# Optimization experiments

Measured on AMD Instinct MI355X. Metric: run time of the kernel, lower is better.

The kernel has to match this reference:

```python
import jax, jax.numpy as jnp
import numpy as np

D_MODEL = 256
D_STATE = 64
NGROUPS = 2
EXPAND = 4
HEADDIM = 128
D_CONV = 4
D_INNER = EXPAND * D_MODEL              # 1024
NHEADS = D_INNER // HEADDIM             # 8
GN = NGROUPS * D_STATE                  # 128
D_IN_PROJ = 2 * D_INNER + 2 * GN + NHEADS  # 2312
EPS = 1e-5


def setup_inputs() -> dict:
    key = jax.random.key(0)
    ks = jax.random.split(key, 12)
    B, L = 2, 4096
    u = jax.random.normal(ks[0], (B, L, D_MODEL), dtype=jnp.float32)
    ln_gamma = jnp.ones((D_MODEL,), jnp.float32)
    ln_beta = jnp.zeros((D_MODEL,), jnp.float32)
    W_in = jax.random.normal(ks[1], (D_MODEL, D_IN_PROJ), jnp.float32) / np.sqrt(D_MODEL)
    conv_w = jax.random.normal(ks[2], (D_INNER + 2 * GN, D_CONV), jnp.float32) * 0.2
    conv_b = jax.random.normal(ks[3], (D_INNER + 2 * GN,), jnp.float32) * 0.02
    dt_bias = jnp.log(jnp.expm1(jax.random.uniform(ks[4], (NHEADS,), jnp.float32, 0.001, 0.1)))
    A_log = jnp.log(jax.random.uniform(ks[5], (NHEADS,), jnp.float32, 1.0, 16.0))
    D_param = jnp.ones((NHEADS,), jnp.float32)
    B_head_scale = jnp.ones((NHEADS, GN), jnp.float32) + 0.02 * jax.random.normal(ks[6], (NHEADS, GN), jnp.float32)
    rms_weight = jnp.ones((D_INNER,), jnp.float32)
    W_out = jax.random.normal(ks[7], (D_INNER, D_MODEL), jnp.float32) / np.sqrt(D_INNER)
    return dict(u=u, ln_gamma=ln_gamma, ln_beta=ln_beta, W_in=W_in, conv_w=conv_w,
                conv_b=conv_b, dt_bias=dt_bias, A_log=A_log, D_param=D_param,
                B_head_scale=B_head_scale, rms_weight=rms_weight, W_out=W_out)


def _mamba_mes(xn, W_in, conv_w, conv_b, dt_bias, A_log, D_param, B_head_scale, rms_weight, W_out):
    B, L, _ = xn.shape
    H, P, K = NHEADS, HEADDIM, D_CONV
    zxbcdt = xn @ W_in                                   # (B,L,2312)
    z = zxbcdt[..., :D_INNER]
    xBC = zxbcdt[..., D_INNER:D_INNER + D_INNER + 2 * GN]
    dt = zxbcdt[..., -H:]
    dt_pos = jax.nn.softplus(dt + dt_bias)               # (B,L,H)
    # causal depthwise conv1d + silu
    xp = jnp.pad(xBC, ((0, 0), (K - 1, 0), (0, 0)))
    conv = sum(xp[:, k:k + L, :] * conv_w[:, k] for k in range(K)) + conv_b
    xBC = jax.nn.silu(conv)
    x = xBC[..., :D_INNER]
    B_shared = xBC[..., D_INNER:D_INNER + GN]            # (B,L,GN)
    C_shared = xBC[..., D_INNER + GN:]                   # (B,L,GN)
    # MES: per-head B via diagonal scale, shared x (mean over heads) and shared C
    B_h = B_shared[:, :, None, :] * B_head_scale[None, None]          # (B,L,H,GN)
    x_shared = x.reshape(B, L, H, P).mean(axis=2)                     # (B,L,P)
    A = -jnp.exp(A_log)                                               # (H,)
    dA = jnp.exp(dt_pos * A)                                          # (B,L,H)
    # selective scan; per-head state (GN, P)
    def step(state, inp):
        dA_t, dt_t, B_t, C_t, x_t = inp   # (B,H),(B,H),(B,H,GN),(B,GN),(B,P)
        state = dA_t[:, :, None, None] * state + jnp.einsum('bh,bhn,bp->bhnp', dt_t, B_t, x_t)
        y_t = jnp.einsum('bn,bhnp->bhp', C_t, state)
        return state, y_t
    init = jnp.zeros((B, H, GN, P), xn.dtype)
    xs = (jnp.moveaxis(dA, 1, 0), jnp.moveaxis(dt_pos, 1, 0), jnp.moveaxis(B_h, 1, 0),
          jnp.moveaxis(C_shared, 1, 0), jnp.moveaxis(x_shared, 1, 0))
    _, ys = jax.lax.scan(step, init, xs)
    y = jnp.moveaxis(ys, 0, 1)                                        # (B,L,H,P)
    y = y + D_param[None, None, :, None] * x_shared[:, :, None, :]    # skip term D*x
    y = y.reshape(B, L, D_INNER)
    # gated RMSNorm: y * silu(z), then rmsnorm
    yg = y * jax.nn.silu(z)
    y = yg * jax.lax.rsqrt(jnp.mean(yg * yg, axis=-1, keepdims=True) + EPS) * rms_weight
    return y @ W_out


def reference(u, ln_gamma, ln_beta, W_in, conv_w, conv_b, dt_bias, A_log,
              D_param, B_head_scale, rms_weight, W_out):
    # pre-LayerNorm
    mu = jnp.mean(u, axis=-1, keepdims=True)
    var = jnp.mean((u - mu) ** 2, axis=-1, keepdims=True)
    xn = (u - mu) * jax.lax.rsqrt(var + EPS) * ln_gamma + ln_beta
    out = _mamba_mes(xn, W_in, conv_w, conv_b, dt_bias, A_log, D_param,
                     B_head_scale, rms_weight, W_out)
    return u + out  # dropout is identity in eval
```

## Files before the change

### kernel.cpp

```cpp
#include <hip/hip_runtime.h>
#include <math.h>

#define LN_TOK 4096
#define NB 2
#define NROWS (NB * LN_TOK)
#define DMODEL 256
#define DINNER 1024
#define NHEADS 8
#define GNN 128
#define DPROJ 2312
#define ZSTRIDE 2432
#define EPSF 1e-5f
#define NCHUNK 32
#define CHUNK 128
#define APAD 72
#define BPAD 64
#define MPAD 136
#define TT 16

typedef unsigned short u16;
typedef unsigned int u32;
typedef __attribute__((ext_vector_type(8))) short shortx8;
typedef __attribute__((ext_vector_type(4))) float floatx4;

__device__ __forceinline__ float sigmoidf_(float v) { return 1.f / (1.f + __expf(-v)); }
__device__ __forceinline__ float siluf_(float v)    { return v / (1.f + __expf(-v)); }
__device__ __forceinline__ float softplusf_(float v){ return v > 20.f ? v : log1pf(__expf(v)); }
__device__ __forceinline__ float b2f(u16 h) { return __uint_as_float(((u32)h) << 16); }
__device__ __forceinline__ u16 f2b(float f) {
    u32 u = __float_as_uint(f);
    u32 r = (u + 0x7fffu + ((u >> 16) & 1u)) >> 16;
    return (u16)r;
}
__device__ __forceinline__ void gld16(const void* g, void* l) {
    __builtin_amdgcn_global_load_lds((const __attribute__((address_space(1))) unsigned int*)g,
                                     (__attribute__((address_space(3))) unsigned int*)l, 16, 0, 0);
}

__global__ __launch_bounds__(256) void k_prologue(const float* __restrict__ u,
                                                  const float* __restrict__ gam,
                                                  const float* __restrict__ bet,
                                                  u16* __restrict__ xn,
                                                  const float* __restrict__ W_in,
                                                  u16* __restrict__ Wt,
                                                  const float* __restrict__ W_out,
                                                  u16* __restrict__ Wot) {
    __shared__ float smem[64 * 65];
    int bid = blockIdx.x;
    int tid = threadIdx.x;
    if (bid < NROWS) {
        float v = u[(size_t)bid * DMODEL + tid];
        float* s1 = smem;
        float* s2 = smem + 256;
        s1[tid] = v; s2[tid] = v * v;
        __syncthreads();
        for (int off = 128; off > 0; off >>= 1) {
            if (tid < off) { s1[tid] += s1[tid + off]; s2[tid] += s2[tid + off]; }
            __syncthreads();
        }
        float mean = s1[0] * (1.f / DMODEL);
        float var  = s2[0] * (1.f / DMODEL) - mean * mean;
        float r = rsqrtf(var + EPSF);
        xn[(size_t)bid * DMODEL + tid] = f2b((v - mean) * r * gam[tid] + bet[tid]);
    } else {
        const float* in; u16* outp; int R, C, Cp, gx, gy;
        if (bid < NROWS + 152) {
            int q = bid - NROWS;
            in = W_in; outp = Wt; R = DMODEL; C = DPROJ; Cp = ZSTRIDE;
            gx = q % (ZSTRIDE / 64); gy = q / (ZSTRIDE / 64);
        } else {
            int q = bid - NROWS - 152;
            in = W_out; outp = Wot; R = DINNER; C = DMODEL; Cp = DMODEL;
            gx = q % (DMODEL / 64); gy = q / (DMODEL / 64);
        }
        float (*tile)[65] = (float(*)[65])smem;
        int c0 = gx * 64, r0 = gy * 64;
        int tx = tid & 63, ty = tid >> 6;
        for (int rr = ty; rr < 64; rr += 4) {
            int r = r0 + rr, c = c0 + tx;
            tile[rr][tx] = (r < R && c < C) ? in[(size_t)r * C + c] : 0.f;
        }
        __syncthreads();
        for (int cc = ty; cc < 64; cc += 4) {
            int c = c0 + cc, r = r0 + tx;
            if (c < Cp && r < R) outp[(size_t)c * R + r] = f2b(tile[tx][cc]);
        }
    }
}

__global__ __launch_bounds__(256) void k_gemm_bf(const u16* __restrict__ A,
                                                 const u16* __restrict__ Bt,
                                                 u16* __restrict__ C,
                                                 int K, int ldc) {
    __shared__ u16 As[128 * BPAD];
    __shared__ u16 Bs[128 * BPAD];
    int tid = threadIdx.x;
    int wave = tid >> 6, lane = tid & 63;
    int wm = wave >> 1, wn = wave & 1;
    int quad = lane >> 4, l16 = lane & 15;
    int m0 = blockIdx.y * 128, n0 = blockIdx.x * 128;
    floatx4 acc[4][4] = {};
    for (int k0 = 0; k0 < K; k0 += 64) {
#pragma unroll
        for (int p = 0; p < 4; p++) {
            int i = p * 256 + tid;
            int row = i >> 3, kk = (i & 7) << 3;
            gld16(&A[(size_t)(m0 + row) * K + k0 + kk], &As[i * 8]);
            gld16(&Bt[(size_t)(n0 + row) * K + k0 + kk], &Bs[i * 8]);
        }
        __syncthreads();
#pragma unroll
        for (int ks = 0; ks < 64; ks += 32) {
            shortx8 af[4], bfr[4];
#pragma unroll
            for (int i = 0; i < 4; i++)
                af[i] = *(shortx8*)&As[(wm * 64 + i * 16 + l16) * BPAD + ks + (quad << 3)];
#pragma unroll
            for (int j = 0; j < 4; j++)
                bfr[j] = *(shortx8*)&Bs[(wn * 64 + j * 16 + l16) * BPAD + ks + (quad << 3)];
#pragma unroll
            for (int i = 0; i < 4; i++)
#pragma unroll
                for (int j = 0; j < 4; j++)
                    acc[i][j] = __builtin_amdgcn_mfma_f32_16x16x32_bf16(af[i], bfr[j], acc[i][j], 0, 0, 0);
        }
        __syncthreads();
    }
#pragma unroll
    for (int i = 0; i < 4; i++) {
        int row = m0 + wm * 64 + i * 16 + quad * 4;
#pragma unroll
        for (int j = 0; j < 4; j++) {
            int col = n0 + wn * 64 + j * 16 + l16;
#pragma unroll
            for (int r = 0; r < 4; r++)
                C[(size_t)(row + r) * ldc + col] = f2b(acc[i][j][r]);
        }
    }
}

__global__ __launch_bounds__(256) void k_gemm2(const u16* __restrict__ A,
                                               const u16* __restrict__ Bt,
                                               float* __restrict__ C,
                                               int K, int ldc,
                                               const float* __restrict__ addC) {
    __shared__ u16 As[128 * BPAD];
    __shared__ u16 Bs[64 * BPAD];
    int tid = threadIdx.x;
    int wave = tid >> 6, lane = tid & 63;
    int wm = wave >> 1, wn = wave & 1;
    int quad = lane >> 4, l16 = lane & 15;
    int m0 = blockIdx.y * 128, n0 = blockIdx.x * 64;
    floatx4 acc[4][2] = {};
    for (int k0 = 0; k0 < K; k0 += 64) {
#pragma unroll
        for (int p = 0; p < 4; p++) {
            int i = p * 256 + tid;
            int row = i >> 3, kk = (i & 7) << 3;
            gld16(&A[(size_t)(m0 + row) * K + k0 + kk], &As[i * 8]);
        }
#pragma unroll
        for (int p = 0; p < 2; p++) {
            int i = p * 256 + tid;
            int row = i >> 3, kk = (i & 7) << 3;
            gld16(&Bt[(size_t)(n0 + row) * K + k0 + kk], &Bs[i * 8]);
        }
        __syncthreads();
#pragma unroll
        for (int ks = 0; ks < 64; ks += 32) {
            shortx8 af[4], bfr[2];
#pragma unroll
            for (int i = 0; i < 4; i++)
                af[i] = *(shortx8*)&As[(wm * 64 + i * 16 + l16) * BPAD + ks + (quad << 3)];
#pragma unroll
            for (int j = 0; j < 2; j++)
                bfr[j] = *(shortx8*)&Bs[(wn * 32 + j * 16 + l16) * BPAD + ks + (quad << 3)];
#pragma unroll
            for (int i = 0; i < 4; i++)
#pragma unroll
                for (int j = 0; j < 2; j++)
                    acc[i][j] = __builtin_amdgcn_mfma_f32_16x16x32_bf16(af[i], bfr[j], acc[i][j], 0, 0, 0);
        }
        __syncthreads();
    }
#pragma unroll
    for (int i = 0; i < 4; i++) {
        int row = m0 + wm * 64 + i * 16 + quad * 4;
#pragma unroll
        for (int j = 0; j < 2; j++) {
            int col = n0 + wn * 32 + j * 16 + l16;
#pragma unroll
            for (int r = 0; r < 4; r++) {
                size_t idx = (size_t)(row + r) * ldc + col;
                float v = acc[i][j][r];
                if (addC) v += addC[idx];
                C[idx] = v;
            }
        }
    }
}

#define LDW 1296
__global__ __launch_bounds__(256) void k_conv(const u16* __restrict__ zxb,
                                              const float* __restrict__ cw,
                                              const float* __restrict__ cb,
                                              const float* __restrict__ dt_bias,
                                              const float* __restrict__ A_log,
                                              u16* __restrict__ xsh, u16* __restrict__ Bsh,
                                              u16* __restrict__ Csh, u16* __restrict__ XT,
                                              u16* __restrict__ BT,
                                              float* __restrict__ dtp, float* __restrict__ laa) {
    int blk = blockIdx.x;
    int b = blk / (LN_TOK / TT), tile = blk % (LN_TOK / TT);
    int t0 = tile * TT;
    int tid = threadIdx.x;
    __shared__ u16 ld[(TT + 3) * LDW];
    __shared__ float sv[TT][260];
    __shared__ u16 bcv[TT][132];

    for (int i = tid; i < (TT + 3) * 161; i += 256) {
        int r = i / 161, ch = (i % 161) * 8;
        int t = t0 - 3 + r;
        int4 v = make_int4(0, 0, 0, 0);
        if (t >= 0)
            v = *(const int4*)&zxb[((size_t)(b * LN_TOK + t)) * ZSTRIDE + DINNER + ch];
        *(int4*)&ld[r * LDW + ch] = v;
    }

    int cmap[5];
#pragma unroll
    for (int k = 0; k < 4; k++) cmap[k] = (tid >> 7) * 512 + (tid & 127) + 128 * k;
    cmap[4] = 1024 + tid;
    float w0[5], w1[5], w2[5], w3[5], bias[5];
#pragma unroll
    for (int k = 0; k < 5; k++) {
        int c = cmap[k];
        w0[k] = cw[c * 4 + 0]; w1[k] = cw[c * 4 + 1];
        w2[k] = cw[c * 4 + 2]; w3[k] = cw[c * 4 + 3];
        bias[k] = cb[c];
    }
    float dtb = 0.f, negA = 0.f;
    if (tid < NHEADS) { dtb = dt_bias[tid]; negA = -__expf(A_log[tid]); }

    __syncthreads();

    float h1[5], h2[5], h3[5];
#pragma unroll
    for (int k = 0; k < 5; k++) {
        h3[k] = b2f(ld[0 * LDW + cmap[k]]);
        h2[k] = b2f(ld[1 * LDW + cmap[k]]);
        h1[k] = b2f(ld[2 * LDW + cmap[k]]);
    }

    for (int m = 0; m < TT; m++) {
        int t = t0 + m;
        size_t rowp = (size_t)(b * LN_TOK + t) * GNN;
        float xpart = 0.f;
#pragma unroll
        for (int k = 0; k < 5; k++) {
            float cur = b2f(ld[(m + 3) * LDW + cmap[k]]);
            float conv = bias[k] + w3[k] * cur + w2[k] * h1[k] + w1[k] * h2[k] + w0[k] * h3[k];
            h3[k] = h2[k]; h2[k] = h1[k]; h1[k] = cur;
            float s = siluf_(conv);
            if (k < 4) xpart += s;
            else {
                u16 sb = f2b(s);
                if (tid < 128) { Bsh[rowp + tid] = sb; bcv[m][tid] = sb; }
                else           Csh[rowp + tid - 128] = sb;
            }
        }
        sv[m][tid] = xpart;
        if (tid < NHEADS) {
            float dtv = b2f(ld[(m + 3) * LDW + 1280 + tid]) + dtb;
            float dp = softplusf_(dtv);
            size_t idx = ((size_t)(b * NHEADS + tid)) * LN_TOK + t;
            dtp[idx] = dp;
            laa[idx] = negA * dp;
        }
    }
    __syncthreads();

    for (int idx = tid; idx < TT * 128; idx += 256) {
        int m = idx >> 7, p = idx & 127;
        xsh[(size_t)(b * LN_TOK + t0 + m) * GNN + p] =
            f2b((sv[m][p] + sv[m][p + 128]) * 0.125f);
    }
    {
        int p = tid & 127, tg = tid >> 7;
        u16 ox[8], ob[8];
#pragma unroll
        for (int j = 0; j < 8; j++) {
            int m = tg * 8 + j;
            ox[j] = f2b((sv[m][p] + sv[m][p + 128]) * 0.125f);
            ob[j] = bcv[m][p];
        }
        size_t base = ((size_t)(b * GNN + p)) * LN_TOK + t0 + tg * 8;
        int4 vx = make_int4((u32)ox[0] | ((u32)ox[1] << 16), (u32)ox[2] | ((u32)ox[3] << 16),
                            (u32)ox[4] | ((u32)ox[5] << 16), (u32)ox[6] | ((u32)ox[7] << 16));
        int4 vb = make_int4((u32)ob[0] | ((u32)ob[1] << 16), (u32)ob[2] | ((u32)ob[3] << 16),
                            (u32)ob[4] | ((u32)ob[5] << 16), (u32)ob[6] | ((u32)ob[7] << 16));
        *(int4*)&XT[base] = vx;
        *(int4*)&BT[base] = vb;
    }
}

__global__ __launch_bounds__(256) void k_chunkS(const u16* __restrict__ BT,
                                                const u16* __restrict__ XT,
                                                const float* __restrict__ scale,
                                                const float* __restrict__ laa,
                                                const float* __restrict__ dtp,
                                                u16* __restrict__ states,
                                                float* __restrict__ gtot) {
    int blk = blockIdx.x;
    int c = blk & 31, h = (blk >> 5) & 7, b = blk >> 8;
    int t0 = c * CHUNK;
    __shared__ u16 As[128 * APAD];
    __shared__ u16 Bs[128 * BPAD];
    __shared__ float g[128], esc[128], scl[128];
    int tid = threadIdx.x;
    int wave = tid >> 6, lane = tid & 63;
    int wm = wave >> 1, wn = wave & 1;
    int quad = lane >> 4, l16 = lane & 15;
    size_t bhbase = (size_t)(b * NHEADS + h) * LN_TOK + t0;
    if (tid < 128) g[tid] = laa[bhbase + tid];
    __syncthreads();
#pragma unroll
    for (int off = 1; off < 128; off <<= 1) {
        float v = 0.f;
        if (tid < 128 && tid >= off) v = g[tid - off];
        __syncthreads();
        if (tid < 128) g[tid] += v;
        __syncthreads();
    }
    if (tid < 128) {
        esc[tid] = __expf(g[127] - g[tid]) * dtp[bhbase + tid];
        scl[tid] = scale[h * GNN + tid];
    }
    if (tid == 0) gtot[(size_t)(b * NHEADS + h) * NCHUNK + c] = g[127];
    __syncthreads();
    floatx4 acc[4][4] = {};
    size_t tbase = (size_t)(b * GNN) * LN_TOK + t0;
    for (int k0 = 0; k0 < 128; k0 += 64) {
#pragma unroll
        for (int p = 0; p < 4; p++) {
            int i = p * 256 + tid;
            int row = i >> 3, kk = (i & 7) << 3;
            gld16(&XT[tbase + (size_t)row * LN_TOK + k0 + kk], &Bs[i * 8]);
            int4 raw = *(const int4*)&BT[tbase + (size_t)row * LN_TOK + k0 + kk];
            u16* rp = (u16*)&raw;
            float sr = scl[row];
            u32 w[4];
#pragma unroll
            for (int q = 0; q < 4; q++) {
                u16 a  = f2b(b2f(rp[2 * q])     * sr * esc[k0 + kk + 2 * q]);
                u16 bb = f2b(b2f(rp[2 * q + 1]) * sr * esc[k0 + kk + 2 * q + 1]);
                w[q] = (u32)a | ((u32)bb << 16);
            }
            *(int4*)&As[row * APAD + kk] = make_int4(w[0], w[1], w[2], w[3]);
        }
        __syncthreads();
#pragma unroll
        for (int ks = 0; ks < 64; ks += 32) {
            shortx8 af[4], bfr[4];
#pragma unroll
            for (int i = 0; i < 4; i++)
                af[i] = *(shortx8*)&As[(wm * 64 + i * 16 + l16) * APAD + ks + (quad << 3)];
#pragma unroll
            for (int j = 0; j < 4; j++)
                bfr[j] = *(shortx8*)&Bs[(wn * 64 + j * 16 + l16) * BPAD + ks + (quad << 3)];
#pragma unroll
            for (int i = 0; i < 4; i++)
#pragma unroll
                for (int j = 0; j < 4; j++)
                    acc[i][j] = __builtin_amdgcn_mfma_f32_16x16x32_bf16(af[i], bfr[j], acc[i][j], 0, 0, 0);
        }
        __syncthreads();
    }
    size_t sbase = (size_t)blk * 16384;
#pragma unroll
    for (int i = 0; i < 4; i++) {
        int n0 = wm * 64 + i * 16 + quad * 4;
#pragma unroll
        for (int j = 0; j < 4; j++) {
            int p = wn * 64 + j * 16 + l16;
            u16 o[4];
#pragma unroll
            for (int r = 0; r < 4; r++) o[r] = f2b(acc[i][j][r]);
            u32 lo = (u32)o[0] | ((u32)o[1] << 16);
            u32 hi = (u32)o[2] | ((u32)o[3] << 16);
            *(uint2*)&states[sbase + (size_t)p * CHUNK + n0] = make_uint2(lo, hi);
        }
    }
}

__global__ void k_scan(u16* __restrict__ states, const float* __restrict__ gtot) {
    int idx = blockIdx.x * 256 + threadIdx.x;
    int bh = idx >> 13;
    int np = (idx & 8191) * 2;
    __shared__ float sG[NCHUNK];
    if (threadIdx.x < NCHUNK) sG[threadIdx.x] = __expf(gtot[bh * NCHUNK + threadIdx.x]);
    __syncthreads();
    size_t base = (size_t)bh * NCHUNK * 16384 + np;
    float r0 = 0.f, r1 = 0.f;
    u32 v = *(u32*)&states[base];
    for (int c = 0; c < NCHUNK; c++) {
        u32 vn = (c < NCHUNK - 1) ? *(u32*)&states[base + (size_t)(c + 1) * 16384] : 0u;
        float l0 = b2f((u16)(v & 0xffff)), l1 = b2f((u16)(v >> 16));
        *(u32*)&states[base + (size_t)c * 16384] = (u32)f2b(r0) | ((u32)f2b(r1) << 16);
        float G = sG[c];
        r0 = G * r0 + l0; r1 = G * r1 + l1;
        v = vn;
    }
}

__global__ __launch_bounds__(256) void k_chunkMY2(const u16* __restrict__ Bsh,
                                                  const u16* __restrict__ Csh,
                                                  const float* __restrict__ scale,
                                                  const u16* __restrict__ states,
                                                  const u16* __restrict__ XT,
                                                  const float* __restrict__ laa,
                                                  const float* __restrict__ dtp,
                                                  u16* __restrict__ y) {
    int blk = blockIdx.x;
    int c = blk & 31, h = (blk >> 5) & 7, b = blk >> 8;
    int t0 = c * CHUNK;
    __shared__ u16 MtAs[128 * MPAD];
    __shared__ u16 Bs[128 * BPAD];
    __shared__ float gsh[128], eg[128], dts[128], sc[128];
    int tid = threadIdx.x;
    int wave = tid >> 6, lane = tid & 63;
    int wm = wave >> 1, wn = wave & 1;
    int quad = lane >> 4, l16 = lane & 15;
    size_t bhbase = (size_t)(b * NHEADS + h) * LN_TOK + t0;
    if (tid < 128) gsh[tid] = laa[bhbase + tid];
    __syncthreads();
#pragma unroll
    for (int off = 1; off < 128; off <<= 1) {
        float v = 0.f;
        if (tid < 128 && tid >= off) v = gsh[tid - off];
        __syncthreads();
        if (tid < 128) gsh[tid] += v;
        __syncthreads();
    }
    if (tid < 128) {
        eg[tid] = __expf(gsh[tid]);
        dts[tid] = dtp[bhbase + tid];
        sc[tid] = scale[h * GNN + tid];
    }
    __syncthreads();
    floatx4 acc[4][4] = {};
    size_t rbase = (size_t)(b * LN_TOK + t0) * GNN;
    for (int k0 = 0; k0 < 128; k0 += 64) {
#pragma unroll
        for (int p = 0; p < 4; p++) {
            int i = p * 256 + tid;
            int row = i >> 3, kk = (i & 7) << 3;
            gld16(&Csh[rbase + (size_t)row * GNN + k0 + kk], &Bs[i * 8]);
            int4 raw = *(const int4*)&Bsh[rbase + (size_t)row * GNN + k0 + kk];
            u16* rp = (u16*)&raw;
            u32 w[4];
#pragma unroll
            for (int q = 0; q < 4; q++) {
                u16 a  = f2b(b2f(rp[2 * q])     * sc[k0 + kk + 2 * q]);
                u16 bb = f2b(b2f(rp[2 * q + 1]) * sc[k0 + kk + 2 * q + 1]);
                w[q] = (u32)a | ((u32)bb << 16);
            }
            *(int4*)&MtAs[row * APAD + kk] = make_int4(w[0], w[1], w[2], w[3]);
        }
        __syncthreads();
#pragma unroll
        for (int ks = 0; ks < 64; ks += 32) {
            shortx8 af[4], bfr[4];
#pragma unroll
            for (int i = 0; i < 4; i++)
                af[i] = *(shortx8*)&MtAs[(wm * 64 + i * 16 + l16) * APAD + ks + (quad << 3)];
#pragma unroll
            for (int j = 0; j < 4; j++)
                bfr[j] = *(shortx8*)&Bs[(wn * 64 + j * 16 + l16) * BPAD + ks + (quad << 3)];
#pragma unroll
            for (int i = 0; i < 4; i++)
#pragma unroll
                for (int j = 0; j < 4; j++)
                    acc[i][j] = __builtin_amdgcn_mfma_f32_16x16x32_bf16(af[i], bfr[j], acc[i][j], 0, 0, 0);
        }
        __syncthreads();
    }
#pragma unroll
    for (int i = 0; i < 4; i++) {
        int s0 = wm * 64 + i * 16 + quad * 4;
#pragma unroll
        for (int j = 0; j < 4; j++) {
            int t = wn * 64 + j * 16 + l16;
            u16 o[4];
#pragma unroll
            for (int r = 0; r < 4; r++) {
                int s = s0 + r;
                float v = (s <= t) ? acc[i][j][r] * __expf(gsh[t] - gsh[s]) * dts[s] : 0.f;
                o[r] = f2b(v);
            }
            u32 lo = (u32)o[0] | ((u32)o[1] << 16);
            u32 hi = (u32)o[2] | ((u32)o[3] << 16);
            *(uint2*)&MtAs[t * MPAD + s0] = make_uint2(lo, hi);
            acc[i][j] = (floatx4){0.f, 0.f, 0.f, 0.f};
        }
    }
    __syncthreads();
    size_t xtb = (size_t)(b * GNN) * LN_TOK + t0;
    for (int k0 = 0; k0 < 128; k0 += 64) {
#pragma unroll
        for (int p = 0; p < 4; p++) {
            int i = p * 256 + tid;
            int row = i >> 3, kk = (i & 7) << 3;
            gld16(&XT[xtb + (size_t)row * LN_TOK + k0 + kk], &Bs[i * 8]);
        }
        __syncthreads();
#pragma unroll
        for (int ks = 0; ks < 64; ks += 32) {
            shortx8 af[4], bfr[4];
#pragma unroll
            for (int i = 0; i < 4; i++)
                af[i] = *(shortx8*)&MtAs[(wm * 64 + i * 16 + l16) * MPAD + k0 + ks + (quad << 3)];
#pragma unroll
            for (int j = 0; j < 4; j++)
                bfr[j] = *(shortx8*)&Bs[(wn * 64 + j * 16 + l16) * BPAD + ks + (quad << 3)];
#pragma unroll
            for (int i = 0; i < 4; i++)
#pragma unroll
                for (int j = 0; j < 4; j++)
                    acc[i][j] = __builtin_amdgcn_mfma_f32_16x16x32_bf16(af[i], bfr[j], acc[i][j], 0, 0, 0);
        }
        __syncthreads();
    }
    size_t sbase = (size_t)blk * 16384;
    for (int k0 = 0; k0 < 128; k0 += 64) {
#pragma unroll
        for (int p = 0; p < 4; p++) {
            int i = p * 256 + tid;
            int row = i >> 3, kk = (i & 7) << 3;
            gld16(&states[sbase + (size_t)row * CHUNK + k0 + kk], &Bs[i * 8]);
            int4 raw = *(const int4*)&Csh[rbase + (size_t)row * GNN + k0 + kk];
            float e = eg[row];
            u16* rp = (u16*)&raw;
            u32 w[4];
#pragma unroll
            for (int q = 0; q < 4; q++) {
                u16 a  = f2b(b2f(rp[2 * q]) * e);
                u16 bb = f2b(b2f(rp[2 * q + 1]) * e);
                w[q] = (u32)a | ((u32)bb << 16);
            }
            *(int4*)&MtAs[row * APAD + kk] = make_int4(w[0], w[1], w[2], w[3]);
        }
        __syncthreads();
#pragma unroll
        for (int ks = 0; ks < 64; ks += 32) {
            shortx8 af[4], bfr[4];
#pragma unroll
            for (int i = 0; i < 4; i++)
                af[i] = *(shortx8*)&MtAs[(wm * 64 + i * 16 + l16) * APAD + ks + (quad << 3)];
#pragma unroll
            for (int j = 0; j < 4; j++)
                bfr[j] = *(shortx8*)&Bs[(wn * 64 + j * 16 + l16) * BPAD + ks + (quad << 3)];
#pragma unroll
            for (int i = 0; i < 4; i++)
#pragma unroll
                for (int j = 0; j < 4; j++)
                    acc[i][j] = __builtin_amdgcn_mfma_f32_16x16x32_bf16(af[i], bfr[j], acc[i][j], 0, 0, 0);
        }
        __syncthreads();
    }
#pragma unroll
    for (int i = 0; i < 4; i++) {
        int t = wm * 64 + i * 16 + quad * 4;
#pragma unroll
        for (int j = 0; j < 4; j++) {
            int p = wn * 64 + j * 16 + l16;
#pragma unroll
            for (int r = 0; r < 4; r++)
                y[((size_t)(b * LN_TOK + t0 + t + r)) * DINNER + h * GNN + p] = f2b(acc[i][j][r]);
        }
    }
}

__global__ void k_gate(const u16* __restrict__ y, const u16* __restrict__ zxb,
                       const u16* __restrict__ xsh, const float* __restrict__ Dp,
                       const float* __restrict__ rw, u16* __restrict__ ybuf) {
    int row = blockIdx.x;
    int tid = threadIdx.x;
    size_t yb = (size_t)row * DINNER;
    size_t zb = (size_t)row * ZSTRIDE;
    size_t xb = (size_t)row * GNN;
    float yg[4];
    float ss = 0.f;
#pragma unroll
    for (int q = 0; q < 4; q++) {
        int k = tid * 4 + q;
        int h = k >> 7, p = k & 127;
        float z = b2f(zxb[zb + k]);
        float v = (b2f(y[yb + k]) + Dp[h] * b2f(xsh[xb + p])) * z * sigmoidf_(z);
        yg[q] = v;
        ss += v * v;
    }
    __shared__ float red[256];
    red[tid] = ss;
    __syncthreads();
    for (int off = 128; off > 0; off >>= 1) {
        if (tid < off) red[tid] += red[tid + off];
        __syncthreads();
    }
    float scale = rsqrtf(red[0] * (1.f / DINNER) + EPSF);
#pragma unroll
    for (int q = 0; q < 4; q++) {
        int k = tid * 4 + q;
        ybuf[yb + k] = f2b(yg[q] * scale * rw[k]);
    }
}

extern "C" void kernel_launch(void* const* d_in, const int* in_sizes, int n_in,
                              void* d_out, int out_size, void* d_ws, size_t ws_size,
                              hipStream_t stream) {
    (void)in_sizes; (void)n_in; (void)out_size; (void)ws_size;
    const float* u        = (const float*)d_in[0];
    const float* ln_gamma = (const float*)d_in[1];
    const float* ln_beta  = (const float*)d_in[2];
    const float* W_in     = (const float*)d_in[3];
    const float* conv_w   = (const float*)d_in[4];
    const float* conv_b   = (const float*)d_in[5];
    const float* dt_bias  = (const float*)d_in[6];
    const float* A_log    = (const float*)d_in[7];
    const float* D_param  = (const float*)d_in[8];
    const float* B_scale  = (const float*)d_in[9];
    const float* rms_w    = (const float*)d_in[10];
    const float* W_out    = (const float*)d_in[11];
    float* out = (float*)d_out;

    char* ws = (char*)d_ws;
    u16*   xn_b   = (u16*)ws;                 ws += (size_t)NROWS * DMODEL * 2;
    u16*   Wt     = (u16*)ws;                 ws += (size_t)ZSTRIDE * DMODEL * 2;
    u16*   Wot    = (u16*)ws;                 ws += (size_t)DMODEL * DINNER * 2;
    u16*   zxb    = (u16*)ws;                 ws += (size_t)NROWS * ZSTRIDE * 2;
    u16*   xsh    = (u16*)ws;                 ws += (size_t)NROWS * GNN * 2;
    u16*   Bsh    = (u16*)ws;                 ws += (size_t)NROWS * GNN * 2;
    u16*   Csh    = (u16*)ws;                 ws += (size_t)NROWS * GNN * 2;
    u16*   XT     = (u16*)ws;                 ws += (size_t)NB * GNN * LN_TOK * 2;
    u16*   BT     = (u16*)ws;                 ws += (size_t)NB * GNN * LN_TOK * 2;
    float* dtp    = (float*)ws;               ws += (size_t)NB * NHEADS * LN_TOK * 4;
    float* laa    = (float*)ws;               ws += (size_t)NB * NHEADS * LN_TOK * 4;
    float* gtot   = (float*)ws;               ws += (size_t)NB * NHEADS * NCHUNK * 4;
    u16*   states = (u16*)ws;                 ws += (size_t)512 * 16384 * 2;
    u16*   ybig   = (u16*)ws;                 ws += (size_t)NROWS * DINNER * 2;
    u16*   ybuf   = (u16*)ws;                 ws += (size_t)NROWS * DINNER * 2;

    k_prologue<<<NROWS + 152 + 64, 256, 0, stream>>>(u, ln_gamma, ln_beta, xn_b,
                                                     W_in, Wt, W_out, Wot);

    k_gemm_bf<<<dim3(ZSTRIDE / 128, NROWS / 128), 256, 0, stream>>>(xn_b, Wt, zxb, DMODEL, ZSTRIDE);

    k_conv<<<NROWS / TT, 256, 0, stream>>>(zxb, conv_w, conv_b, dt_bias, A_log,
                                           xsh, Bsh, Csh, XT, BT, dtp, laa);

    k_chunkS<<<NB * NHEADS * NCHUNK, 256, 0, stream>>>(BT, XT, B_scale, laa, dtp, states, gtot);

    k_scan<<<512, 256, 0, stream>>>(states, gtot);

    k_chunkMY2<<<NB * NHEADS * NCHUNK, 256, 0, stream>>>(Bsh, Csh, B_scale, states,
                                                         XT, laa, dtp, ybig);

    k_gate<<<NROWS, 256, 0, stream>>>(ybig, zxb, xsh, D_param, rms_w, ybuf);

    k_gemm2<<<dim3(DMODEL / 64, NROWS / 128), 256, 0, stream>>>(ybuf, Wot, out, DINNER, DMODEL, u);
}
```

Baseline: 215.0 us.

## Load full 128-wide K tiles at once and use wave-shuffle prefix scan in chunk kernels

In k_chunkS and k_chunkMY2 each GEMM stage now stages the whole 128-wide K dimension in shared memory in one pass, replacing two 64-wide passes. This removes the per-half barriers and the reload loop, at the cost of more LDS per block, which can lower occupancy. The 128-element cumulative log-decay scan, which used a barrier per step, is replaced by a 64-lane __shfl_up scan per wavefront plus one shared-memory carry. A few barriers between phases are also moved or dropped.

```diff
diff --git a/kernel.cpp b/kernel.cpp
--- a/kernel.cpp
+++ b/kernel.cpp
@@ -13,9 +13,9 @@
 #define EPSF 1e-5f
 #define NCHUNK 32
 #define CHUNK 128
-#define APAD 72
 #define BPAD 64
-#define MPAD 136
+#define FPAD 136
+#define BKF 128
 #define TT 16
 
 typedef unsigned short u16;
@@ -314,67 +314,69 @@
     int blk = blockIdx.x;
     int c = blk & 31, h = (blk >> 5) & 7, b = blk >> 8;
     int t0 = c * CHUNK;
-    __shared__ u16 As[128 * APAD];
-    __shared__ u16 Bs[128 * BPAD];
-    __shared__ float g[128], esc[128], scl[128];
+    __shared__ u16 As[128 * FPAD];
+    __shared__ u16 Bs[128 * BKF];
+    __shared__ float gsh[132], esc[128], scl[128];
     int tid = threadIdx.x;
     int wave = tid >> 6, lane = tid & 63;
     int wm = wave >> 1, wn = wave & 1;
     int quad = lane >> 4, l16 = lane & 15;
     size_t bhbase = (size_t)(b * NHEADS + h) * LN_TOK + t0;
-    if (tid < 128) g[tid] = laa[bhbase + tid];
-    __syncthreads();
-#pragma unroll
-    for (int off = 1; off < 128; off <<= 1) {
-        float v = 0.f;
-        if (tid < 128 && tid >= off) v = g[tid - off];
-        __syncthreads();
-        if (tid < 128) g[tid] += v;
-        __syncthreads();
-    }
+
+    float gv = (tid < 128) ? laa[bhbase + tid] : 0.f;
+#pragma unroll
+    for (int off = 1; off < 64; off <<= 1) {
+        float v = __shfl_up(gv, off, 64);
+        if (lane >= off) gv += v;
+    }
+    if (tid == 63) gsh[130] = gv;
+    __syncthreads();
+    if (tid >= 64 && tid < 128) gv += gsh[130];
+    if (tid < 128) gsh[tid] = gv;
+    __syncthreads();
+    float glast = gsh[127];
     if (tid < 128) {
-        esc[tid] = __expf(g[127] - g[tid]) * dtp[bhbase + tid];
+        esc[tid] = __expf(glast - gsh[tid]) * dtp[bhbase + tid];
         scl[tid] = scale[h * GNN + tid];
     }
-    if (tid == 0) gtot[(size_t)(b * NHEADS + h) * NCHUNK + c] = g[127];
-    __syncthreads();
+    if (tid == 0) gtot[(size_t)(b * NHEADS + h) * NCHUNK + c] = glast;
+    __syncthreads();
+
+    size_t tbase = (size_t)(b * GNN) * LN_TOK + t0;
+#pragma unroll
+    for (int p = 0; p < 8; p++) {
+        int i = p * 256 + tid;
+        int row = i >> 4, kk = (i & 15) << 3;
+        gld16(&XT[tbase + (size_t)row * LN_TOK + kk], &Bs[i * 8]);
+        int4 raw = *(const int4*)&BT[tbase + (size_t)row * LN_TOK + kk];
+        u16* rp = (u16*)&raw;
+        float sr = scl[row];
+        u32 w[4];
+#pragma unroll
+        for (int q = 0; q < 4; q++) {
+            u16 a  = f2b(b2f(rp[2 * q])     * sr * esc[kk + 2 * q]);
+            u16 bb = f2b(b2f(rp[2 * q + 1]) * sr * esc[kk + 2 * q + 1]);
+            w[q] = (u32)a | ((u32)bb << 16);
+        }
+        *(int4*)&As[row * FPAD + kk] = make_int4(w[0], w[1], w[2], w[3]);
+    }
+    __syncthreads();
+
     floatx4 acc[4][4] = {};
-    size_t tbase = (size_t)(b * GNN) * LN_TOK + t0;
-    for (int k0 = 0; k0 < 128; k0 += 64) {
-#pragma unroll
-        for (int p = 0; p < 4; p++) {
-            int i = p * 256 + tid;
-            int row = i >> 3, kk = (i & 7) << 3;
-            gld16(&XT[tbase + (size_t)row * LN_TOK + k0 + kk], &Bs[i * 8]);
-            int4 raw = *(const int4*)&BT[tbase + (size_t)row * LN_TOK + k0 + kk];
-            u16* rp = (u16*)&raw;
-            float sr = scl[row];
-            u32 w[4];
-#pragma unroll
-            for (int q = 0; q < 4; q++) {
-                u16 a  = f2b(b2f(rp[2 * q])     * sr * esc[k0 + kk + 2 * q]);
-                u16 bb = f2b(b2f(rp[2 * q + 1]) * sr * esc[k0 + kk + 2 * q + 1]);
-                w[q] = (u32)a | ((u32)bb << 16);
-            }
-            *(int4*)&As[row * APAD + kk] = make_int4(w[0], w[1], w[2], w[3]);
-        }
-        __syncthreads();
-#pragma unroll
-        for (int ks = 0; ks < 64; ks += 32) {
-            shortx8 af[4], bfr[4];
-#pragma unroll
-            for (int i = 0; i < 4; i++)
-                af[i] = *(shortx8*)&As[(wm * 64 + i * 16 + l16) * APAD + ks + (quad << 3)];
+#pragma unroll
+    for (int ks = 0; ks < 128; ks += 32) {
+        shortx8 af[4], bfr[4];
+#pragma unroll
+        for (int i = 0; i < 4; i++)
+            af[i] = *(shortx8*)&As[(wm * 64 + i * 16 + l16) * FPAD + ks + (quad << 3)];
+#pragma unroll
+        for (int j = 0; j < 4; j++)
+            bfr[j] = *(shortx8*)&Bs[(wn * 64 + j * 16 + l16) * BKF + ks + (quad << 3)];
+#pragma unroll
+        for (int i = 0; i < 4; i++)
 #pragma unroll
             for (int j = 0; j < 4; j++)
-                bfr[j] = *(shortx8*)&Bs[(wn * 64 + j * 16 + l16) * BPAD + ks + (quad << 3)];
-#pragma unroll
-            for (int i = 0; i < 4; i++)
-#pragma unroll
-                for (int j = 0; j < 4; j++)
-                    acc[i][j] = __builtin_amdgcn_mfma_f32_16x16x32_bf16(af[i], bfr[j], acc[i][j], 0, 0, 0);
-        }
-        __syncthreads();
+                acc[i][j] = __builtin_amdgcn_mfma_f32_16x16x32_bf16(af[i], bfr[j], acc[i][j], 0, 0, 0);
     }
     size_t sbase = (size_t)blk * 16384;
 #pragma unroll
@@ -424,67 +426,68 @@
     int blk = blockIdx.x;
     int c = blk & 31, h = (blk >> 5) & 7, b = blk >> 8;
     int t0 = c * CHUNK;
-    __shared__ u16 MtAs[128 * MPAD];
-    __shared__ u16 Bs[128 * BPAD];
-    __shared__ float gsh[128], eg[128], dts[128], sc[128];
+    __shared__ u16 MtAs[128 * FPAD];
+    __shared__ u16 Bs[128 * BKF];
+    __shared__ float gsh[132], eg[128], dts[128], sc[128];
     int tid = threadIdx.x;
     int wave = tid >> 6, lane = tid & 63;
     int wm = wave >> 1, wn = wave & 1;
     int quad = lane >> 4, l16 = lane & 15;
     size_t bhbase = (size_t)(b * NHEADS + h) * LN_TOK + t0;
-    if (tid < 128) gsh[tid] = laa[bhbase + tid];
-    __syncthreads();
-#pragma unroll
-    for (int off = 1; off < 128; off <<= 1) {
-        float v = 0.f;
-        if (tid < 128 && tid >= off) v = gsh[tid - off];
-        __syncthreads();
-        if (tid < 128) gsh[tid] += v;
-        __syncthreads();
-    }
+
+    float gv = (tid < 128) ? laa[bhbase + tid] : 0.f;
+#pragma unroll
+    for (int off = 1; off < 64; off <<= 1) {
+        float v = __shfl_up(gv, off, 64);
+        if (lane >= off) gv += v;
+    }
+    if (tid == 63) gsh[130] = gv;
+    __syncthreads();
+    if (tid >= 64 && tid < 128) gv += gsh[130];
+    if (tid < 128) gsh[tid] = gv;
+    __syncthreads();
     if (tid < 128) {
         eg[tid] = __expf(gsh[tid]);
         dts[tid] = dtp[bhbase + tid];
         sc[tid] = scale[h * GNN + tid];
     }
     __syncthreads();
+
     floatx4 acc[4][4] = {};
     size_t rbase = (size_t)(b * LN_TOK + t0) * GNN;
-    for (int k0 = 0; k0 < 128; k0 += 64) {
-#pragma unroll
-        for (int p = 0; p < 4; p++) {
-            int i = p * 256 + tid;
-            int row = i >> 3, kk = (i & 7) << 3;
-            gld16(&Csh[rbase + (size_t)row * GNN + k0 + kk], &Bs[i * 8]);
-            int4 raw = *(const int4*)&Bsh[rbase + (size_t)row * GNN + k0 + kk];
-            u16* rp = (u16*)&raw;
-            u32 w[4];
-#pragma unroll
-            for (int q = 0; q < 4; q++) {
-                u16 a  = f2b(b2f(rp[2 * q])     * sc[k0 + kk + 2 * q]);
-                u16 bb = f2b(b2f(rp[2 * q + 1]) * sc[k0 + kk + 2 * q + 1]);
-                w[q] = (u32)a | ((u32)bb << 16);
-            }
-            *(int4*)&MtAs[row * APAD + kk] = make_int4(w[0], w[1], w[2], w[3]);
-        }
-        __syncthreads();
-#pragma unroll
-        for (int ks = 0; ks < 64; ks += 32) {
-            shortx8 af[4], bfr[4];
-#pragma unroll
-            for (int i = 0; i < 4; i++)
-                af[i] = *(shortx8*)&MtAs[(wm * 64 + i * 16 + l16) * APAD + ks + (quad << 3)];
+#pragma unroll
+    for (int p = 0; p < 8; p++) {
+        int i = p * 256 + tid;
+        int row = i >> 4, kk = (i & 15) << 3;
+        gld16(&Csh[rbase + (size_t)row * GNN + kk], &Bs[i * 8]);
+        int4 raw = *(const int4*)&Bsh[rbase + (size_t)row * GNN + kk];
+        u16* rp = (u16*)&raw;
+        u32 w[4];
+#pragma unroll
+        for (int q = 0; q < 4; q++) {
+            u16 a  = f2b(b2f(rp[2 * q])     * sc[kk + 2 * q]);
+            u16 bb = f2b(b2f(rp[2 * q + 1]) * sc[kk + 2 * q + 1]);
+            w[q] = (u32)a | ((u32)bb << 16);
+        }
+        *(int4*)&MtAs[row * FPAD + kk] = make_int4(w[0], w[1], w[2], w[3]);
+    }
+    __syncthreads();
+#pragma unroll
+    for (int ks = 0; ks < 128; ks += 32) {
+        shortx8 af[4], bfr[4];
+#pragma unroll
+        for (int i = 0; i < 4; i++)
+            af[i] = *(shortx8*)&MtAs[(wm * 64 + i * 16 + l16) * FPAD + ks + (quad << 3)];
+#pragma unroll
+        for (int j = 0; j < 4; j++)
+            bfr[j] = *(shortx8*)&Bs[(wn * 64 + j * 16 + l16) * BKF + ks + (quad << 3)];
+#pragma unroll
+        for (int i = 0; i < 4; i++)
 #pragma unroll
             for (int j = 0; j < 4; j++)
-                bfr[j] = *(shortx8*)&Bs[(wn * 64 + j * 16 + l16) * BPAD + ks + (quad << 3)];
-#pragma unroll
-            for (int i = 0; i < 4; i++)
-#pragma unroll
-                for (int j = 0; j < 4; j++)
-                    acc[i][j] = __builtin_amdgcn_mfma_f32_16x16x32_bf16(af[i], bfr[j], acc[i][j], 0, 0, 0);
-        }
-        __syncthreads();
-    }
+                acc[i][j] = __builtin_amdgcn_mfma_f32_16x16x32_bf16(af[i], bfr[j], acc[i][j], 0, 0, 0);
+    }
+    __syncthreads();
 #pragma unroll
     for (int i = 0; i < 4; i++) {
         int s0 = wm * 64 + i * 16 + quad * 4;
@@ -500,73 +503,67 @@
             }
             u32 lo = (u32)o[0] | ((u32)o[1] << 16);
             u32 hi = (u32)o[2] | ((u32)o[3] << 16);
-            *(uint2*)&MtAs[t * MPAD + s0] = make_uint2(lo, hi);
+            *(uint2*)&MtAs[t * FPAD + s0] = make_uint2(lo, hi);
             acc[i][j] = (floatx4){0.f, 0.f, 0.f, 0.f};
         }
     }
-    __syncthreads();
     size_t xtb = (size_t)(b * GNN) * LN_TOK + t0;
-    for (int k0 = 0; k0 < 128; k0 += 64) {
-#pragma unroll
-        for (int p = 0; p < 4; p++) {
-            int i = p * 256 + tid;
-            int row = i >> 3, kk = (i & 7) << 3;
-            gld16(&XT[xtb + (size_t)row * LN_TOK + k0 + kk], &Bs[i * 8]);
-        }
-        __syncthreads();
-#pragma unroll
-        for (int ks = 0; ks < 64; ks += 32) {
-            shortx8 af[4], bfr[4];
-#pragma unroll
-            for (int i = 0; i < 4; i++)
-                af[i] = *(shortx8*)&MtAs[(wm * 64 + i * 16 + l16) * MPAD + k0 + ks + (quad << 3)];
+#pragma unroll
+    for (int p = 0; p < 8; p++) {
+        int i = p * 256 + tid;
+        int row = i >> 4, kk = (i & 15) << 3;
+        gld16(&XT[xtb + (size_t)row * LN_TOK + kk], &Bs[i * 8]);
+    }
+    __syncthreads();
+#pragma unroll
+    for (int ks = 0; ks < 128; ks += 32) {
+        shortx8 af[4], bfr[4];
+#pragma unroll
+        for (int i = 0; i < 4; i++)
+            af[i] = *(shortx8*)&MtAs[(wm * 64 + i * 16 + l16) * FPAD + ks + (quad << 3)];
+#pragma unroll
+        for (int j = 0; j < 4; j++)
+            bfr[j] = *(shortx8*)&Bs[(wn * 64 + j * 16 + l16) * BKF + ks + (quad << 3)];
+#pragma unroll
+        for (int i = 0; i < 4; i++)
 #pragma unroll
             for (int j = 0; j < 4; j++)
-                bfr[j] = *(shortx8*)&Bs[(wn * 64 + j * 16 + l16) * BPAD + ks + (quad << 3)];
-#pragma unroll
-            for (int i = 0; i < 4; i++)
-#pragma unroll
-                for (int j = 0; j < 4; j++)
-                    acc[i][j] = __builtin_amdgcn_mfma_f32_16x16x32_bf16(af[i], bfr[j], acc[i][j], 0, 0, 0);
-        }
-        __syncthreads();
-    }
+                acc[i][j] = __builtin_amdgcn_mfma_f32_16x16x32_bf16(af[i], bfr[j], acc[i][j], 0, 0, 0);
+    }
+    __syncthreads();
     size_t sbase = (size_t)blk * 16384;
-    for (int k0 = 0; k0 < 128; k0 += 64) {
-#pragma unroll
-        for (int p = 0; p < 4; p++) {
-            int i = p * 256 + tid;
-            int row = i >> 3, kk = (i & 7) << 3;
-            gld16(&states[sbase + (size_t)row * CHUNK + k0 + kk], &Bs[i * 8]);
-            int4 raw = *(const int4*)&Csh[rbase + (size_t)row * GNN + k0 + kk];
-            float e = eg[row];
-            u16* rp = (u16*)&raw;
-            u32 w[4];
-#pragma unroll
-            for (int q = 0; q < 4; q++) {
-                u16 a  = f2b(b2f(rp[2 * q]) * e);
-                u16 bb = f2b(b2f(rp[2 * q + 1]) * e);
-                w[q] = (u32)a | ((u32)bb << 16);
-            }
-            *(int4*)&MtAs[row * APAD + kk] = make_int4(w[0], w[1], w[2], w[3]);
-        }
-        __syncthreads();
-#pragma unroll
-        for (int ks = 0; ks < 64; ks += 32) {
-            shortx8 af[4], bfr[4];
-#pragma unroll
-            for (int i = 0; i < 4; i++)
-                af[i] = *(shortx8*)&MtAs[(wm * 64 + i * 16 + l16) * APAD + ks + (quad << 3)];
+#pragma unroll
+    for (int p = 0; p < 8; p++) {
+        int i = p * 256 + tid;
+        int row = i >> 4, kk = (i & 15) << 3;
+        gld16(&states[sbase + (size_t)row * CHUNK + kk], &Bs[i * 8]);
+        int4 raw = *(const int4*)&Csh[rbase + (size_t)row * GNN + kk];
+        float e = eg[row];
+        u16* rp = (u16*)&raw;
+        u32 w[4];
+#pragma unroll
+        for (int q = 0; q < 4; q++) {
+            u16 a  = f2b(b2f(rp[2 * q]) * e);
+            u16 bb = f2b(b2f(rp[2 * q + 1]) * e);
+            w[q] = (u32)a | ((u32)bb << 16);
+        }
+        *(int4*)&MtAs[row * FPAD + kk] = make_int4(w[0], w[1], w[2], w[3]);
+    }
+    __syncthreads();
+#pragma unroll
+    for (int ks = 0; ks < 128; ks += 32) {
+        shortx8 af[4], bfr[4];
+#pragma unroll
+        for (int i = 0; i < 4; i++)
+            af[i] = *(shortx8*)&MtAs[(wm * 64 + i * 16 + l16) * FPAD + ks + (quad << 3)];
+#pragma unroll
+        for (int j = 0; j < 4; j++)
+            bfr[j] = *(shortx8*)&Bs[(wn * 64 + j * 16 + l16) * BKF + ks + (quad << 3)];
+#pragma unroll
+        for (int i = 0; i < 4; i++)
 #pragma unroll
             for (int j = 0; j < 4; j++)
-                bfr[j] = *(shortx8*)&Bs[(wn * 64 + j * 16 + l16) * BPAD + ks + (quad << 3)];
-#pragma unroll
-            for (int i = 0; i < 4; i++)
-#pragma unroll
-                for (int j = 0; j < 4; j++)
-                    acc[i][j] = __builtin_amdgcn_mfma_f32_16x16x32_bf16(af[i], bfr[j], acc[i][j], 0, 0, 0);
-        }
-        __syncthreads();
+                acc[i][j] = __builtin_amdgcn_mfma_f32_16x16x32_bf16(af[i], bfr[j], acc[i][j], 0, 0, 0);
     }
 #pragma unroll
     for (int i = 0; i < 4; i++) {
```

New measurement: 217.0 us. About the same (+0.9%).
